# Optimization experiments

Hardware: AMD Instinct MI355X
Metric: run time of the kernel (lower is better)

The kernel has to match this reference:

```python
import jax, jax.numpy as jnp
import numpy as np

B, F, V, E, D1, DD, L2 = 4096, 32, 50000, 64, 256, 16, 128


def setup_inputs() -> dict:
    key = jax.random.key(0)
    ks = jax.random.split(key, 16)
    s = 0.05  # small init scale to keep tanh unsaturated
    return {
        "sparse": jax.random.randint(ks[0], (B, F), 0, V, dtype=jnp.int32),
        "dense": jax.random.normal(ks[1], (B, DD), dtype=jnp.float32),
        "tables": jax.random.normal(ks[2], (F, V, E), dtype=jnp.float32) * s,
        "Wz": jax.random.normal(ks[3], (D1, F, E), dtype=jnp.float32) * s,
        "bz": jnp.zeros((D1,), jnp.float32),
        "Wpi": jax.random.normal(ks[4], (D1, F, F), dtype=jnp.float32) * s,
        "bpi": jnp.zeros((D1,), jnp.float32),
        "Wpo": jax.random.normal(ks[5], (D1, E, E), dtype=jnp.float32) * s,
        "bpo": jnp.zeros((D1,), jnp.float32),
        "B1": jax.random.normal(ks[6], (D1,), dtype=jnp.float32) * s,
        "W1": jax.random.normal(ks[7], (D1 + DD, D1), dtype=jnp.float32) * s,
        "b1": jnp.zeros((D1,), jnp.float32),
        "W2": jax.random.normal(ks[8], (D1, L2), dtype=jnp.float32) * s,
        "b2": jnp.zeros((L2,), jnp.float32),
        "W3": jax.random.normal(ks[9], (L2, 1), dtype=jnp.float32) * s,
        "b3": jnp.zeros((1,), jnp.float32),
    }


def reference(sparse, dense, tables, Wz, bz, Wpi, bpi, Wpo, bpo, B1,
              W1, b1, W2, b2, W3, b3):
    # Embedding lookup: per-field table gather -> [B, F, E]
    emb = tables[jnp.arange(F)[None, :], sparse]
    # Lz: Conv1d(in=F, kernel=E) over [B, F, E] == full contraction -> [B, D1]
    Lz = jnp.einsum('bfe,dfe->bd', emb, Wz) + bz
    # Inner product: [B, F, F], then Conv1d(in=F, kernel=F) full contraction
    inner = jnp.einsum('bie,bje->bij', emb, emb)
    Lp_inner = jnp.einsum('bij,dij->bd', inner, Wpi) + bpi
    # Outer product: sum_{i,j} x_i^T x_j == s^T s with s = sum_i x_i (exact rewrite)
    s = emb.sum(axis=1)                      # [B, E]
    outer = s[:, :, None] * s[:, None, :]    # [B, E, E]
    Lp_outer = jnp.einsum('bij,dij->bd', outer, Wpo) + bpo
    L1 = Lz + Lp_inner + Lp_outer + B1       # [B, D1]
    deep_x = jnp.concatenate([L1, dense], axis=1)  # [B, D1+DD]
    h = jnp.tanh(deep_x @ W1 + b1)
    h = jnp.tanh(h @ W2 + b2)
    out = (h @ W3 + b3)[:, 0]                # [B]
    return out
```

## Files before the change

kernel.cpp:

```cpp
#include <hip/hip_runtime.h>
#include <hip/hip_bf16.h>

#define B_    4096
#define F_    32
#define V_    50000
#define E_    64
#define D1_   256
#define DD_   16
#define L2N_  128
#define KX    3072
#define KTOT  7168

typedef __bf16 bf16x8 __attribute__((ext_vector_type(8)));
typedef float  f32x4  __attribute__((ext_vector_type(4)));

typedef __attribute__((address_space(1))) const void gvoid;
typedef __attribute__((address_space(3))) void svoid;

__device__ __forceinline__ ushort f2b(float f){
  __bf16 h = (__bf16)f; return __builtin_bit_cast(ushort, h);
}
__device__ __forceinline__ float b2f(ushort u){
  return __uint_as_float(((uint)u) << 16);
}
__device__ __forceinline__ void gload16(const void* g, void* l){
  __builtin_amdgcn_global_load_lds((gvoid*)g, (svoid*)l, 16, 0, 0);
}

__global__ __launch_bounds__(256) void prep_gather(
    const float* __restrict__ Wz, const float* __restrict__ Wpi,
    const float* __restrict__ Wpo, const float* __restrict__ W1,
    const float* __restrict__ W2,
    const int* __restrict__ sparse, const float* __restrict__ tables,
    ushort* __restrict__ WBb, ushort* __restrict__ W1b, ushort* __restrict__ W2b,
    ushort* __restrict__ Xb, ushort* __restrict__ Sb) {
  int bid = blockIdx.x, t = threadIdx.x;
  if (bid < 640) {
    if (bid < 256) {
      int n = bid;
#pragma unroll
      for (int j = 0; j < 7; ++j) {
        int k4 = (j * 256 + t) * 4;
        float4 v;
        if (k4 < 2048)      v = *(const float4*)&Wz [(size_t)n * 2048 + k4];
        else if (k4 < 3072) v = *(const float4*)&Wpi[(size_t)n * 1024 + (k4 - 2048)];
        else                v = *(const float4*)&Wpo[(size_t)n * 4096 + (k4 - 3072)];
        ushort4 o = make_ushort4(f2b(v.x), f2b(v.y), f2b(v.z), f2b(v.w));
        *(ushort4*)&WBb[(size_t)n * KTOT + k4] = o;
      }
    } else if (bid < 512) {
      int n = bid - 256;
      float v0 = (t < 272) ? W1[(size_t)t * 256 + n] : 0.f;
      W1b[(size_t)n * 288 + t] = f2b(v0);
      if (t < 32) {
        int k2 = 256 + t;
        float v1 = (k2 < 272) ? W1[(size_t)k2 * 256 + n] : 0.f;
        W1b[(size_t)n * 288 + k2] = f2b(v1);
      }
    } else {
      int n = bid - 512;
      W2b[(size_t)n * 256 + t] = f2b(W2[(size_t)t * 128 + n]);
    }
    return;
  }

  int w = t >> 6, l = t & 63;
  int b = (bid - 640) * 4 + w;
  int fr = l & 15, q = l >> 4;

  int i0 = sparse[b * F_ + fr];
  int i1 = sparse[b * F_ + 16 + fr];
  const float* r0 = tables + ((size_t)fr * V_ + i0) * 64;
  const float* r1 = tables + ((size_t)(16 + fr) * V_ + i1) * 64;

  float4 v[2][2][2];
#pragma unroll
  for (int ks = 0; ks < 2; ++ks) {
    v[0][ks][0] = *(const float4*)(r0 + ks * 32 + q * 8);
    v[0][ks][1] = *(const float4*)(r0 + ks * 32 + q * 8 + 4);
    v[1][ks][0] = *(const float4*)(r1 + ks * 32 + q * 8);
    v[1][ks][1] = *(const float4*)(r1 + ks * 32 + q * 8 + 4);
  }

  bf16x8 fg[2][2];
#pragma unroll
  for (int rh = 0; rh < 2; ++rh)
#pragma unroll
    for (int ks = 0; ks < 2; ++ks) {
      bf16x8 a;
      a[0] = (__bf16)v[rh][ks][0].x; a[1] = (__bf16)v[rh][ks][0].y;
      a[2] = (__bf16)v[rh][ks][0].z; a[3] = (__bf16)v[rh][ks][0].w;
      a[4] = (__bf16)v[rh][ks][1].x; a[5] = (__bf16)v[rh][ks][1].y;
      a[6] = (__bf16)v[rh][ks][1].z; a[7] = (__bf16)v[rh][ks][1].w;
      fg[rh][ks] = a;
      *(bf16x8*)&Xb[(size_t)b * KX + (rh * 16 + fr) * 64 + ks * 32 + q * 8] = a;
    }

  float sv[2][8];
#pragma unroll
  for (int ks = 0; ks < 2; ++ks) {
    sv[ks][0] = v[0][ks][0].x + v[1][ks][0].x; sv[ks][1] = v[0][ks][0].y + v[1][ks][0].y;
    sv[ks][2] = v[0][ks][0].z + v[1][ks][0].z; sv[ks][3] = v[0][ks][0].w + v[1][ks][0].w;
    sv[ks][4] = v[0][ks][1].x + v[1][ks][1].x; sv[ks][5] = v[0][ks][1].y + v[1][ks][1].y;
    sv[ks][6] = v[0][ks][1].z + v[1][ks][1].z; sv[ks][7] = v[0][ks][1].w + v[1][ks][1].w;
  }
#pragma unroll
  for (int m = 1; m < 16; m <<= 1)
#pragma unroll
    for (int ks = 0; ks < 2; ++ks)
#pragma unroll
      for (int j = 0; j < 8; ++j)
        sv[ks][j] += __shfl_xor(sv[ks][j], m, 64);
  if (fr == 0) {
#pragma unroll
    for (int ks = 0; ks < 2; ++ks) {
      ushort4 o0 = make_ushort4(f2b(sv[ks][0]), f2b(sv[ks][1]), f2b(sv[ks][2]), f2b(sv[ks][3]));
      ushort4 o1 = make_ushort4(f2b(sv[ks][4]), f2b(sv[ks][5]), f2b(sv[ks][6]), f2b(sv[ks][7]));
      *(ushort4*)&Sb[(size_t)b * 64 + ks * 32 + q * 8]     = o0;
      *(ushort4*)&Sb[(size_t)b * 64 + ks * 32 + q * 8 + 4] = o1;
    }
  }

  f32x4 g[2][2] = {};
#pragma unroll
  for (int ks = 0; ks < 2; ++ks)
#pragma unroll
    for (int ri = 0; ri < 2; ++ri)
#pragma unroll
      for (int rj = 0; rj < 2; ++rj)
        g[ri][rj] = __builtin_amdgcn_mfma_f32_16x16x32_bf16(
            fg[ri][ks], fg[rj][ks], g[ri][rj], 0, 0, 0);

#pragma unroll
  for (int ri = 0; ri < 2; ++ri)
#pragma unroll
    for (int rj = 0; rj < 2; ++rj)
#pragma unroll
      for (int r = 0; r < 4; ++r) {
        int rowi = ri * 16 + q * 4 + r;
        int colj = rj * 16 + fr;
        Xb[(size_t)b * KX + 2048 + rowi * 32 + colj] = f2b(g[ri][rj][r]);
      }
}

#define BMg 128
#define BNg 128
__global__ __launch_bounds__(256, 1) void gemm_l1(
    const ushort* __restrict__ Xb, const ushort* __restrict__ WBb,
    const ushort* __restrict__ Sb, float* __restrict__ Lp) {
  __shared__ __align__(16) ushort As[2][BMg * 64];
  __shared__ __align__(16) ushort Bs[2][BNg * 64];
  __shared__ __align__(16) ushort Ssb[BMg * 72];

  int bid = blockIdx.x;
  int lg  = (bid & 7) * 32 + (bid >> 3);
  int kc  = lg >> 6;
  int nT  = (lg >> 5) & 1;
  int mT  = lg & 31;
  int bRow = mT * BMg, n0 = nT * BNg;

  int tid = threadIdx.x, w = tid >> 6, l = tid & 63;
  int wm = (w >> 1) * 64, wn = (w & 1) * 64;

#pragma unroll
  for (int p = 0; p < 4; ++p) {
    int idx = p * 2048 + tid * 8;
    int row = idx >> 6, c = idx & 63;
    *(uint4*)&Ssb[row * 72 + c] = *(const uint4*)&Sb[(size_t)bRow * 64 + idx];
  }

  float sregf[4][16];
#pragma unroll
  for (int mi = 0; mi < 4; ++mi) {
    const ushort* base = Sb + (size_t)(bRow + wm + mi * 16 + (l & 15)) * 64 + (l >> 4) * 8;
    ushort4 a0 = *(const ushort4*)(base);
    ushort4 a1 = *(const ushort4*)(base + 4);
    ushort4 b0 = *(const ushort4*)(base + 32);
    ushort4 b1 = *(const ushort4*)(base + 36);
    sregf[mi][0] = b2f(a0.x); sregf[mi][1] = b2f(a0.y); sregf[mi][2] = b2f(a0.z); sregf[mi][3] = b2f(a0.w);
    sregf[mi][4] = b2f(a1.x); sregf[mi][5] = b2f(a1.y); sregf[mi][6] = b2f(a1.z); sregf[mi][7] = b2f(a1.w);
    sregf[mi][8]  = b2f(b0.x); sregf[mi][9]  = b2f(b0.y); sregf[mi][10] = b2f(b0.z); sregf[mi][11] = b2f(b0.w);
    sregf[mi][12] = b2f(b1.x); sregf[mi][13] = b2f(b1.y); sregf[mi][14] = b2f(b1.z); sregf[mi][15] = b2f(b1.w);
  }

  int r8 = l >> 3;
  int sg = ((l & 7) ^ r8) * 8;

  auto stageA = [&](int bI, int kt) {
    const ushort* src = Xb + (size_t)(bRow + w * 32 + r8) * KX + kt * 64 + sg;
#pragma unroll
    for (int c = 0; c < 4; ++c)
      gload16(src + (size_t)(c * 8) * KX, &As[bI][(w * 32 + c * 8) * 64]);
  };
  auto stageB = [&](int bI, int kt) {
    const ushort* src = WBb + (size_t)(n0 + w * 32 + r8) * KTOT + kt * 64 + sg;
#pragma unroll
    for (int c = 0; c < 4; ++c)
      gload16(src + (size_t)(c * 8) * KTOT, &Bs[bI][(w * 32 + c * 8) * 64]);
  };

  f32x4 acc[4][4] = {};
  bf16x8 af[4][2], bf[4][2];
  int buf = 0;

  int kt0 = kc * 12;
  stageA(0, kt0); stageB(0, kt0);
  __syncthreads();
  for (int t = 0; t < 12; ++t) {
    if (t + 1 < 12) { stageA(buf ^ 1, kt0 + t + 1); stageB(buf ^ 1, kt0 + t + 1); }
#pragma unroll
    for (int mi = 0; mi < 4; ++mi) {
      int row = wm + mi * 16 + (l & 15);
#pragma unroll
      for (int ks = 0; ks < 2; ++ks) {
        int slot = (ks * 4 + (l >> 4)) ^ (row & 7);
        af[mi][ks] = *(const bf16x8*)&As[buf][row * 64 + slot * 8];
      }
    }
#pragma unroll
    for (int ni = 0; ni < 4; ++ni) {
      int col = wn + ni * 16 + (l & 15);
#pragma unroll
      for (int ks = 0; ks < 2; ++ks) {
        int slot = (ks * 4 + (l >> 4)) ^ (col & 7);
        bf[ni][ks] = *(const bf16x8*)&Bs[buf][col * 64 + slot * 8];
      }
    }
#pragma unroll
    for (int ks = 0; ks < 2; ++ks)
#pragma unroll
      for (int mi = 0; mi < 4; ++mi)
#pragma unroll
        for (int ni = 0; ni < 4; ++ni)
          acc[mi][ni] = __builtin_amdgcn_mfma_f32_16x16x32_bf16(
              af[mi][ks], bf[ni][ks], acc[mi][ni], 0, 0, 0);
    __syncthreads();
    buf ^= 1;
  }

  int i0 = kc * 16;
  stageB(buf, 48 + i0);
  __syncthreads();
  for (int t = 0; t < 16; ++t) {
    if (t + 1 < 16) stageB(buf ^ 1, 48 + i0 + t + 1);
    int i = i0 + t;
#pragma unroll
    for (int mi = 0; mi < 4; ++mi) {
      int row = wm + mi * 16 + (l & 15);
      float si = b2f(Ssb[row * 72 + i]);
#pragma unroll
      for (int ks = 0; ks < 2; ++ks) {
        bf16x8 a;
#pragma unroll
        for (int j = 0; j < 8; ++j)
          a[j] = (__bf16)(si * sregf[mi][ks * 8 + j]);
        af[mi][ks] = a;
      }
    }
#pragma unroll
    for (int ni = 0; ni < 4; ++ni) {
      int col = wn + ni * 16 + (l & 15);
#pragma unroll
      for (int ks = 0; ks < 2; ++ks) {
        int slot = (ks * 4 + (l >> 4)) ^ (col & 7);
        bf[ni][ks] = *(const bf16x8*)&Bs[buf][col * 64 + slot * 8];
      }
    }
#pragma unroll
    for (int ks = 0; ks < 2; ++ks)
#pragma unroll
      for (int mi = 0; mi < 4; ++mi)
#pragma unroll
        for (int ni = 0; ni < 4; ++ni)
          acc[mi][ni] = __builtin_amdgcn_mfma_f32_16x16x32_bf16(
              af[mi][ks], bf[ni][ks], acc[mi][ni], 0, 0, 0);
    __syncthreads();
    buf ^= 1;
  }

  float* Lpk = Lp + (size_t)kc * (B_ * D1_);
#pragma unroll
  for (int mi = 0; mi < 4; ++mi) {
    int row0 = bRow + wm + mi * 16 + (l >> 4) * 4;
#pragma unroll
    for (int ni = 0; ni < 4; ++ni) {
      int col = n0 + wn + ni * 16 + (l & 15);
#pragma unroll
      for (int r = 0; r < 4; ++r)
        Lpk[(size_t)(row0 + r) * D1_ + col] = acc[mi][ni][r];
    }
  }
}

__global__ __launch_bounds__(256) void mlp_fused(
    const float* __restrict__ Lp, const float* __restrict__ dense,
    const ushort* __restrict__ W1b, const ushort* __restrict__ W2b,
    const float* __restrict__ bz, const float* __restrict__ bpi,
    const float* __restrict__ bpo, const float* __restrict__ B1v,
    const float* __restrict__ b1, const float* __restrict__ b2,
    const float* __restrict__ W3, const float* __restrict__ b3,
    float* __restrict__ out) {
  __shared__ ushort hs[16 * 264];
  __shared__ ushort h2s[16 * 136];
  __shared__ float bvs[256];
  int b0 = blockIdx.x * 16;
  int tid = threadIdx.x, w = tid >> 6, l = tid & 63;
  int row = l & 15, q = l >> 4;
  int wn = w * 64;

  bvs[tid] = bz[tid] + bpi[tid] + bpo[tid] + B1v[tid];
  __syncthreads();

  f32x4 acc1[4] = {};
  const float* L0 = Lp;
  const float* L1p = Lp + (size_t)B_ * D1_;
  const float* L2p = Lp + (size_t)2 * B_ * D1_;
  const float* L3p = Lp + (size_t)3 * B_ * D1_;
  for (int kt = 0; kt < 9; ++kt) {
    int k0 = kt * 32 + q * 8;
    bf16x8 afr;
    if (kt < 8) {
      size_t base = (size_t)(b0 + row) * D1_ + k0;
      float4 s0 = *(const float4*)&L0[base];
      float4 s1 = *(const float4*)&L0[base + 4];
      float4 u;
      u = *(const float4*)&L1p[base];     s0.x+=u.x; s0.y+=u.y; s0.z+=u.z; s0.w+=u.w;
      u = *(const float4*)&L1p[base + 4]; s1.x+=u.x; s1.y+=u.y; s1.z+=u.z; s1.w+=u.w;
      u = *(const float4*)&L2p[base];     s0.x+=u.x; s0.y+=u.y; s0.z+=u.z; s0.w+=u.w;
      u = *(const float4*)&L2p[base + 4]; s1.x+=u.x; s1.y+=u.y; s1.z+=u.z; s1.w+=u.w;
      u = *(const float4*)&L3p[base];     s0.x+=u.x; s0.y+=u.y; s0.z+=u.z; s0.w+=u.w;
      u = *(const float4*)&L3p[base + 4]; s1.x+=u.x; s1.y+=u.y; s1.z+=u.z; s1.w+=u.w;
      float4 bv0 = *(const float4*)&bvs[k0];
      float4 bv1 = *(const float4*)&bvs[k0 + 4];
      afr[0] = (__bf16)(s0.x + bv0.x); afr[1] = (__bf16)(s0.y + bv0.y);
      afr[2] = (__bf16)(s0.z + bv0.z); afr[3] = (__bf16)(s0.w + bv0.w);
      afr[4] = (__bf16)(s1.x + bv1.x); afr[5] = (__bf16)(s1.y + bv1.y);
      afr[6] = (__bf16)(s1.z + bv1.z); afr[7] = (__bf16)(s1.w + bv1.w);
    } else if (q < 2) {
      float4 u0 = *(const float4*)&dense[(size_t)(b0 + row) * DD_ + q * 8];
      float4 u1 = *(const float4*)&dense[(size_t)(b0 + row) * DD_ + q * 8 + 4];
      afr[0] = (__bf16)u0.x; afr[1] = (__bf16)u0.y; afr[2] = (__bf16)u0.z; afr[3] = (__bf16)u0.w;
      afr[4] = (__bf16)u1.x; afr[5] = (__bf16)u1.y; afr[6] = (__bf16)u1.z; afr[7] = (__bf16)u1.w;
    } else {
      afr = (bf16x8)(__bf16)0.f;
    }
#pragma unroll
    for (int ni = 0; ni < 4; ++ni) {
      bf16x8 bfr = *(const bf16x8*)&W1b[(size_t)(wn + ni * 16 + row) * 288 + k0];
      acc1[ni] = __builtin_amdgcn_mfma_f32_16x16x32_bf16(afr, bfr, acc1[ni], 0, 0, 0);
    }
  }
#pragma unroll
  for (int ni = 0; ni < 4; ++ni) {
    int col = wn + ni * 16 + row;
    float bias = b1[col];
#pragma unroll
    for (int r = 0; r < 4; ++r)
      hs[(q * 4 + r) * 264 + col] = f2b(tanhf(acc1[ni][r] + bias));
  }
  __syncthreads();

  int wn2 = w * 32;
  f32x4 acc2[2] = {};
  for (int kt = 0; kt < 8; ++kt) {
    int k0 = kt * 32 + q * 8;
    bf16x8 afr = *(const bf16x8*)&hs[row * 264 + k0];
#pragma unroll
    for (int ni = 0; ni < 2; ++ni) {
      bf16x8 bfr = *(const bf16x8*)&W2b[(size_t)(wn2 + ni * 16 + row) * 256 + k0];
      acc2[ni] = __builtin_amdgcn_mfma_f32_16x16x32_bf16(afr, bfr, acc2[ni], 0, 0, 0);
    }
  }
#pragma unroll
  for (int ni = 0; ni < 2; ++ni) {
    int col = wn2 + ni * 16 + row;
    float bias = b2[col];
#pragma unroll
    for (int r = 0; r < 4; ++r)
      h2s[(q * 4 + r) * 136 + col] = f2b(tanhf(acc2[ni][r] + bias));
  }
  __syncthreads();

  if (w == 0) {
    int rr = l >> 2, g = l & 3;
    float sum = 0.f;
#pragma unroll
    for (int jj = 0; jj < 32; ++jj) {
      int j = g * 32 + jj;
      sum += b2f(h2s[rr * 136 + j]) * W3[j];
    }
    sum += __shfl_xor(sum, 1, 64);
    sum += __shfl_xor(sum, 2, 64);
    if (g == 0) out[b0 + rr] = sum + b3[0];
  }
}

extern "C" void kernel_launch(void* const* d_in, const int* in_sizes, int n_in,
                              void* d_out, int out_size, void* d_ws, size_t ws_size,
                              hipStream_t stream) {
  const int*   sparse = (const int*)  d_in[0];
  const float* dense  = (const float*)d_in[1];
  const float* tables = (const float*)d_in[2];
  const float* Wz     = (const float*)d_in[3];
  const float* bz     = (const float*)d_in[4];
  const float* Wpi    = (const float*)d_in[5];
  const float* bpi    = (const float*)d_in[6];
  const float* Wpo    = (const float*)d_in[7];
  const float* bpo    = (const float*)d_in[8];
  const float* B1v    = (const float*)d_in[9];
  const float* W1     = (const float*)d_in[10];
  const float* b1     = (const float*)d_in[11];
  const float* W2     = (const float*)d_in[12];
  const float* b2     = (const float*)d_in[13];
  const float* W3     = (const float*)d_in[14];
  const float* b3     = (const float*)d_in[15];
  float* out = (float*)d_out;

  char* ws = (char*)d_ws;
  ushort* Xb  = (ushort*)(ws);
  ushort* WBb = (ushort*)(ws + 25165824);
  ushort* W1b = (ushort*)(ws + 28835840);
  ushort* W2b = (ushort*)(ws + 28983296);
  ushort* Sb  = (ushort*)(ws + 29048832);
  float*  Lp  = (float*) (ws + 29573120);

  prep_gather<<<dim3(1664), dim3(256), 0, stream>>>(
      Wz, Wpi, Wpo, W1, W2, sparse, tables, WBb, W1b, W2b, Xb, Sb);
  gemm_l1    <<<dim3(256),  dim3(256), 0, stream>>>(Xb, WBb, Sb, Lp);
  mlp_fused  <<<dim3(256),  dim3(256), 0, stream>>>(
      Lp, dense, W1b, W2b, bz, bpi, bpo, B1v, b1, b2, W3, b3, out);
}
```

Before: 70.42 us.

## Load GEMM operands straight to registers, interleave X and outer-product K steps

```diff
diff --git a/kernel.cpp b/kernel.cpp
--- a/kernel.cpp
+++ b/kernel.cpp
@@ -14,18 +14,14 @@
 typedef __bf16 bf16x8 __attribute__((ext_vector_type(8)));
 typedef float  f32x4  __attribute__((ext_vector_type(4)));
 
-typedef __attribute__((address_space(1))) const void gvoid;
-typedef __attribute__((address_space(3))) void svoid;
-
 __device__ __forceinline__ ushort f2b(float f){
   __bf16 h = (__bf16)f; return __builtin_bit_cast(ushort, h);
 }
 __device__ __forceinline__ float b2f(ushort u){
   return __uint_as_float(((uint)u) << 16);
 }
-__device__ __forceinline__ void gload16(const void* g, void* l){
-  __builtin_amdgcn_global_load_lds((gvoid*)g, (svoid*)l, 16, 0, 0);
-}
+__device__ __forceinline__ float blo(uint u){ return __uint_as_float(u << 16); }
+__device__ __forceinline__ float bhi(uint u){ return __uint_as_float(u & 0xffff0000u); }
 
 __global__ __launch_bounds__(256) void prep_gather(
     const float* __restrict__ Wz, const float* __restrict__ Wpi,
@@ -143,139 +139,114 @@
       }
 }
 
-#define BMg 128
-#define BNg 128
 __global__ __launch_bounds__(256, 1) void gemm_l1(
     const ushort* __restrict__ Xb, const ushort* __restrict__ WBb,
     const ushort* __restrict__ Sb, float* __restrict__ Lp) {
-  __shared__ __align__(16) ushort As[2][BMg * 64];
-  __shared__ __align__(16) ushort Bs[2][BNg * 64];
-  __shared__ __align__(16) ushort Ssb[BMg * 72];
+  __shared__ ushort Ssl[128 * 18];
 
   int bid = blockIdx.x;
-  int lg  = (bid & 7) * 32 + (bid >> 3);
-  int kc  = lg >> 6;
-  int nT  = (lg >> 5) & 1;
-  int mT  = lg & 31;
-  int bRow = mT * BMg, n0 = nT * BNg;
+  int xcd = bid & 7, idx = bid >> 3;
+  int kc  = xcd >> 1;
+  int mT  = (xcd & 1) * 16 + (idx >> 1);
+  int nT  = idx & 1;
+  int bRow = mT * 128, n0 = nT * 128;
 
   int tid = threadIdx.x, w = tid >> 6, l = tid & 63;
   int wm = (w >> 1) * 64, wn = (w & 1) * 64;
-
-#pragma unroll
-  for (int p = 0; p < 4; ++p) {
-    int idx = p * 2048 + tid * 8;
-    int row = idx >> 6, c = idx & 63;
-    *(uint4*)&Ssb[row * 72 + c] = *(const uint4*)&Sb[(size_t)bRow * 64 + idx];
-  }
-
-  float sregf[4][16];
+  int fr = l & 15, q = l >> 4;
+
+#pragma unroll
+  for (int r = 0; r < 8; ++r) {
+    int p = r * 256 + tid;
+    int row = p >> 4, col = p & 15;
+    Ssl[row * 18 + col] = Sb[(size_t)(bRow + row) * 64 + kc * 16 + col];
+  }
+  __syncthreads();
+
+  uint4 sregu[4][2];
+  const ushort* Ab[4];
+  const ushort* Bb[4];
 #pragma unroll
   for (int mi = 0; mi < 4; ++mi) {
-    const ushort* base = Sb + (size_t)(bRow + wm + mi * 16 + (l & 15)) * 64 + (l >> 4) * 8;
-    ushort4 a0 = *(const ushort4*)(base);
-    ushort4 a1 = *(const ushort4*)(base + 4);
-    ushort4 b0 = *(const ushort4*)(base + 32);
-    ushort4 b1 = *(const ushort4*)(base + 36);
-    sregf[mi][0] = b2f(a0.x); sregf[mi][1] = b2f(a0.y); sregf[mi][2] = b2f(a0.z); sregf[mi][3] = b2f(a0.w);
-    sregf[mi][4] = b2f(a1.x); sregf[mi][5] = b2f(a1.y); sregf[mi][6] = b2f(a1.z); sregf[mi][7] = b2f(a1.w);
-    sregf[mi][8]  = b2f(b0.x); sregf[mi][9]  = b2f(b0.y); sregf[mi][10] = b2f(b0.z); sregf[mi][11] = b2f(b0.w);
-    sregf[mi][12] = b2f(b1.x); sregf[mi][13] = b2f(b1.y); sregf[mi][14] = b2f(b1.z); sregf[mi][15] = b2f(b1.w);
-  }
-
-  int r8 = l >> 3;
-  int sg = ((l & 7) ^ r8) * 8;
-
-  auto stageA = [&](int bI, int kt) {
-    const ushort* src = Xb + (size_t)(bRow + w * 32 + r8) * KX + kt * 64 + sg;
-#pragma unroll
-    for (int c = 0; c < 4; ++c)
-      gload16(src + (size_t)(c * 8) * KX, &As[bI][(w * 32 + c * 8) * 64]);
+    int grow = bRow + wm + mi * 16 + fr;
+    sregu[mi][0] = *(const uint4*)&Sb[(size_t)grow * 64 + q * 8];
+    sregu[mi][1] = *(const uint4*)&Sb[(size_t)grow * 64 + 32 + q * 8];
+    Ab[mi] = Xb + (size_t)grow * KX + kc * 768 + q * 8;
+  }
+#pragma unroll
+  for (int ni = 0; ni < 4; ++ni)
+    Bb[ni] = WBb + (size_t)(n0 + wn + ni * 16 + fr) * KTOT + q * 8;
+
+  f32x4 acc[4][4] = {};
+  bf16x8 afb[2][4][2], bfb[2][4][2];
+
+  auto loadA = [&](int buf, int xt) {
+#pragma unroll
+    for (int mi = 0; mi < 4; ++mi)
+#pragma unroll
+      for (int ks = 0; ks < 2; ++ks)
+        afb[buf][mi][ks] = *(const bf16x8*)(Ab[mi] + xt * 64 + ks * 32);
   };
-  auto stageB = [&](int bI, int kt) {
-    const ushort* src = WBb + (size_t)(n0 + w * 32 + r8) * KTOT + kt * 64 + sg;
-#pragma unroll
-    for (int c = 0; c < 4; ++c)
-      gload16(src + (size_t)(c * 8) * KTOT, &Bs[bI][(w * 32 + c * 8) * 64]);
+  auto loadB = [&](int buf, int bkt) {
+#pragma unroll
+    for (int ni = 0; ni < 4; ++ni)
+#pragma unroll
+      for (int ks = 0; ks < 2; ++ks)
+        bfb[buf][ni][ks] = *(const bf16x8*)(Bb[ni] + bkt * 64 + ks * 32);
   };
 
-  f32x4 acc[4][4] = {};
-  bf16x8 af[4][2], bf[4][2];
-  int buf = 0;
-
-  int kt0 = kc * 12;
-  stageA(0, kt0); stageB(0, kt0);
-  __syncthreads();
-  for (int t = 0; t < 12; ++t) {
-    if (t + 1 < 12) { stageA(buf ^ 1, kt0 + t + 1); stageB(buf ^ 1, kt0 + t + 1); }
-#pragma unroll
-    for (int mi = 0; mi < 4; ++mi) {
-      int row = wm + mi * 16 + (l & 15);
-#pragma unroll
-      for (int ks = 0; ks < 2; ++ks) {
-        int slot = (ks * 4 + (l >> 4)) ^ (row & 7);
-        af[mi][ks] = *(const bf16x8*)&As[buf][row * 64 + slot * 8];
+  loadA(0, 0);
+  loadB(0, kc * 12);
+
+#pragma unroll
+  for (int s = 0; s < 28; ++s) {
+    const bool isX = (s < 24) && ((s & 1) == 0);
+    const int  xt  = s >> 1;
+    const int  ou  = (s < 24) ? (s >> 1) : (s - 12);
+
+    if (s + 1 < 28) {
+      const int ns = s + 1;
+      const bool nX = (ns < 24) && ((ns & 1) == 0);
+      const int nbkt = nX ? (kc * 12 + (ns >> 1))
+                          : (48 + kc * 16 + ((ns < 24) ? (ns >> 1) : (ns - 12)));
+      loadB(ns & 1, nbkt);
+    }
+    if (isX && (xt + 1) < 12) loadA((xt + 1) & 1, xt + 1);
+
+    if (isX) {
+#pragma unroll
+      for (int ks = 0; ks < 2; ++ks)
+#pragma unroll
+        for (int mi = 0; mi < 4; ++mi)
+#pragma unroll
+          for (int ni = 0; ni < 4; ++ni)
+            acc[mi][ni] = __builtin_amdgcn_mfma_f32_16x16x32_bf16(
+                afb[xt & 1][mi][ks], bfb[s & 1][ni][ks], acc[mi][ni], 0, 0, 0);
+    } else {
+      bf16x8 afs[4][2];
+#pragma unroll
+      for (int mi = 0; mi < 4; ++mi) {
+        float si = b2f(Ssl[(wm + mi * 16 + fr) * 18 + ou]);
+#pragma unroll
+        for (int ks = 0; ks < 2; ++ks) {
+          uint4 uv = sregu[mi][ks];
+          bf16x8 a;
+          a[0] = (__bf16)(si * blo(uv.x)); a[1] = (__bf16)(si * bhi(uv.x));
+          a[2] = (__bf16)(si * blo(uv.y)); a[3] = (__bf16)(si * bhi(uv.y));
+          a[4] = (__bf16)(si * blo(uv.z)); a[5] = (__bf16)(si * bhi(uv.z));
+          a[6] = (__bf16)(si * blo(uv.w)); a[7] = (__bf16)(si * bhi(uv.w));
+          afs[mi][ks] = a;
+        }
       }
-    }
-#pragma unroll
-    for (int ni = 0; ni < 4; ++ni) {
-      int col = wn + ni * 16 + (l & 15);
-#pragma unroll
-      for (int ks = 0; ks < 2; ++ks) {
-        int slot = (ks * 4 + (l >> 4)) ^ (col & 7);
-        bf[ni][ks] = *(const bf16x8*)&Bs[buf][col * 64 + slot * 8];
-      }
-    }
-#pragma unroll
-    for (int ks = 0; ks < 2; ++ks)
-#pragma unroll
-      for (int mi = 0; mi < 4; ++mi)
-#pragma unroll
-        for (int ni = 0; ni < 4; ++ni)
-          acc[mi][ni] = __builtin_amdgcn_mfma_f32_16x16x32_bf16(
-              af[mi][ks], bf[ni][ks], acc[mi][ni], 0, 0, 0);
-    __syncthreads();
-    buf ^= 1;
-  }
-
-  int i0 = kc * 16;
-  stageB(buf, 48 + i0);
-  __syncthreads();
-  for (int t = 0; t < 16; ++t) {
-    if (t + 1 < 16) stageB(buf ^ 1, 48 + i0 + t + 1);
-    int i = i0 + t;
-#pragma unroll
-    for (int mi = 0; mi < 4; ++mi) {
-      int row = wm + mi * 16 + (l & 15);
-      float si = b2f(Ssb[row * 72 + i]);
-#pragma unroll
-      for (int ks = 0; ks < 2; ++ks) {
-        bf16x8 a;
-#pragma unroll
-        for (int j = 0; j < 8; ++j)
-          a[j] = (__bf16)(si * sregf[mi][ks * 8 + j]);
-        af[mi][ks] = a;
-      }
-    }
-#pragma unroll
-    for (int ni = 0; ni < 4; ++ni) {
-      int col = wn + ni * 16 + (l & 15);
-#pragma unroll
-      for (int ks = 0; ks < 2; ++ks) {
-        int slot = (ks * 4 + (l >> 4)) ^ (col & 7);
-        bf[ni][ks] = *(const bf16x8*)&Bs[buf][col * 64 + slot * 8];
-      }
-    }
-#pragma unroll
-    for (int ks = 0; ks < 2; ++ks)
-#pragma unroll
-      for (int mi = 0; mi < 4; ++mi)
-#pragma unroll
-        for (int ni = 0; ni < 4; ++ni)
-          acc[mi][ni] = __builtin_amdgcn_mfma_f32_16x16x32_bf16(
-              af[mi][ks], bf[ni][ks], acc[mi][ni], 0, 0, 0);
-    __syncthreads();
-    buf ^= 1;
+#pragma unroll
+      for (int ks = 0; ks < 2; ++ks)
+#pragma unroll
+        for (int mi = 0; mi < 4; ++mi)
+#pragma unroll
+          for (int ni = 0; ni < 4; ++ni)
+            acc[mi][ni] = __builtin_amdgcn_mfma_f32_16x16x32_bf16(
+                afs[mi][ks], bfb[s & 1][ni][ks], acc[mi][ni], 0, 0, 0);
+    }
   }
 
   float* Lpk = Lp + (size_t)kc * (B_ * D1_);
@@ -284,7 +255,7 @@
     int row0 = bRow + wm + mi * 16 + (l >> 4) * 4;
 #pragma unroll
     for (int ni = 0; ni < 4; ++ni) {
-      int col = n0 + wn + ni * 16 + (l & 15);
+      int col = n0 + wn + ni * 16 + fr;
 #pragma unroll
       for (int r = 0; r < 4; ++r)
         Lpk[(size_t)(row0 + r) * D1_ + col] = acc[mi][ni][r];
@@ -312,7 +283,7 @@
   __syncthreads();
 
   f32x4 acc1[4] = {};
-  const float* L0 = Lp;
+  const float* L0  = Lp;
   const float* L1p = Lp + (size_t)B_ * D1_;
   const float* L2p = Lp + (size_t)2 * B_ * D1_;
   const float* L3p = Lp + (size_t)3 * B_ * D1_;
```

New measurement: 82.44 us. +17.1%, slower.
